# Optimization experiments

Measured on AMD Instinct MI355X. Metric: run time of the kernel, lower is better.

## Reference

```python
import jax, jax.numpy as jnp
import numpy as np

N_M = 100000  # musicians
N_T = 100000  # tracks
E = 400000
D = 128


def _sage(x_src, x_dst, edge, W_l, b_l, W_r, n_dst):
    """PyG SAGEConv: lin_l(mean_{j in N(i)} x_src[j]) + lin_r(x_dst[i])."""
    src, dst = edge[0], edge[1]
    msg = x_src[src]                                   # [E, D] gather
    agg = jax.ops.segment_sum(msg, dst, num_segments=n_dst)
    cnt = jax.ops.segment_sum(jnp.ones((edge.shape[1],), x_src.dtype), dst,
                              num_segments=n_dst)
    agg = agg / jnp.maximum(cnt, 1.0)[:, None]         # mean aggregation
    return agg @ W_l.T + b_l + x_dst @ W_r.T


def setup_inputs() -> dict:
    key = jax.random.key(0)
    ks = jax.random.split(key, 7)
    scale = 0.05
    return {
        "x_m": jax.random.normal(ks[0], (N_M, D), jnp.float32),
        "x_t": jax.random.normal(ks[1], (N_T, D), jnp.float32),
        "Wl": jax.random.normal(ks[2], (3, 2, D, D), jnp.float32) * scale,
        "bl": jnp.zeros((3, 2, D), jnp.float32),
        "Wr": jax.random.normal(ks[3], (3, 2, D, D), jnp.float32) * scale,
        "edge_mt": jax.random.randint(ks[4], (2, E), 0, N_T, jnp.int32).astype(jnp.int64),
        "edge_tm": jax.random.randint(ks[5], (2, E), 0, N_M, jnp.int32).astype(jnp.int64),
    }


def reference(x_m, x_t, Wl, bl, Wr, edge_mt, edge_tm):
    # 3 HeteroConv(SAGEConv) layers; dropout=0.0 is identity.
    for layer in range(3):
        # edge type 0: musician -plays_on-> track  (dst = track)
        new_t = _sage(x_m, x_t, edge_mt, Wl[layer, 0], bl[layer, 0], Wr[layer, 0], N_T)
        # edge type 1: track -features-> musician  (dst = musician)
        new_m = _sage(x_t, x_m, edge_tm, Wl[layer, 1], bl[layer, 1], Wr[layer, 1], N_M)
        if layer < 2:
            new_m = jax.nn.relu(new_m)
            new_t = jax.nn.relu(new_t)
        x_m, x_t = new_m, new_t
    return x_m, x_t
```

## Files before the change

kernel.cpp:

```cpp
#include <hip/hip_runtime.h>
#include <hip/hip_bf16.h>

typedef __bf16 bf16_t;
typedef __attribute__((ext_vector_type(4))) __bf16 bf16x4;
typedef __attribute__((ext_vector_type(8))) __bf16 bf16x8;
typedef __attribute__((ext_vector_type(4))) float f32x4;

#define DIM 128
#define GTILE 32

__device__ __forceinline__ void gl_lds16(const void* g, void* l) {
    __builtin_amdgcn_global_load_lds(
        (const __attribute__((address_space(1))) unsigned int*)g,
        (__attribute__((address_space(3))) unsigned int*)l, 16, 0, 0);
}

__global__ void prep_count(const float* __restrict__ Wl, const float* __restrict__ Wr,
                           bf16_t* __restrict__ Wc,
                           const int* __restrict__ dA, int* __restrict__ cA,
                           const int* __restrict__ dB, int* __restrict__ cB,
                           int E, int PB) {
    int blk = blockIdx.x;
    if (blk < PB) {
        int idx = blk * 256 + threadIdx.x;
        if (idx >= 6 * 128 * 256) return;
        int k = idx & 255;
        int n = (idx >> 8) & 127;
        int s = idx >> 15;
        float v;
        if (k < 128) v = Wl[((size_t)s * 128 + n) * 128 + k];
        else         v = Wr[((size_t)s * 128 + n) * 128 + (k - 128)];
        Wc[idx] = (bf16_t)v;
    } else {
        int i = (blk - PB) * 256 + threadIdx.x;
        if (i < E) atomicAdd(&cA[dA[i]], 1);
        else if (i < 2 * E) atomicAdd(&cB[dB[i - E]], 1);
    }
}

__global__ __launch_bounds__(256) void scan_local2(
    const int* __restrict__ cntA, int* __restrict__ partA, int* __restrict__ bsumA,
    int MA, int NBA,
    const int* __restrict__ cntB, int* __restrict__ partB, int* __restrict__ bsumB,
    int MB) {
    int blk = blockIdx.x;
    const int* cnt; int* partial; int* blocksum; int M; int b;
    if (blk < NBA) { cnt = cntA; partial = partA; blocksum = bsumA; M = MA; b = blk; }
    else           { cnt = cntB; partial = partB; blocksum = bsumB; M = MB; b = blk - NBA; }
    __shared__ int sdata[256];
    int i = b * 256 + threadIdx.x;
    int v = (i < M) ? cnt[i] : 0;
    sdata[threadIdx.x] = v;
    __syncthreads();
    for (int off = 1; off < 256; off <<= 1) {
        int t = (threadIdx.x >= off) ? sdata[threadIdx.x - off] : 0;
        __syncthreads();
        sdata[threadIdx.x] += t;
        __syncthreads();
    }
    int incl = sdata[threadIdx.x];
    if (i < M) partial[i] = incl - v;
    if (threadIdx.x == 255) blocksum[b] = incl;
}

__global__ __launch_bounds__(256) void scan_blocks2(int* __restrict__ bsA, int NA,
                                                    int* __restrict__ bsB, int NBcnt) {
    int* blocksum = blockIdx.x ? bsB : bsA;
    int NB = blockIdx.x ? NBcnt : NA;
    __shared__ int sdata[256];
    __shared__ int running;
    if (threadIdx.x == 0) running = 0;
    __syncthreads();
    for (int base = 0; base < NB; base += 256) {
        int i = base + threadIdx.x;
        int v = (i < NB) ? blocksum[i] : 0;
        sdata[threadIdx.x] = v;
        __syncthreads();
        for (int off = 1; off < 256; off <<= 1) {
            int t = (threadIdx.x >= off) ? sdata[threadIdx.x - off] : 0;
            __syncthreads();
            sdata[threadIdx.x] += t;
            __syncthreads();
        }
        int incl = sdata[threadIdx.x];
        int r = running;
        __syncthreads();
        if (i < NB) blocksum[i] = incl - v + r;
        if (threadIdx.x == 0) running = r + sdata[255];
        __syncthreads();
    }
}

__global__ __launch_bounds__(256) void add_offsets2(
    const int* __restrict__ pA, const int* __restrict__ bsA,
    int* __restrict__ rsA, int* __restrict__ curA, int MA, int NBA,
    const int* __restrict__ pB, const int* __restrict__ bsB,
    int* __restrict__ rsB, int* __restrict__ curB, int MB) {
    int blk = blockIdx.x;
    const int *partial, *blocksum; int *rowstart, *cursor; int M, b;
    if (blk < NBA) { partial = pA; blocksum = bsA; rowstart = rsA; cursor = curA; M = MA; b = blk; }
    else           { partial = pB; blocksum = bsB; rowstart = rsB; cursor = curB; M = MB; b = blk - NBA; }
    int i = b * 256 + threadIdx.x;
    if (i < M) {
        int rs = partial[i] + blocksum[i >> 8];
        rowstart[i] = rs;
        cursor[i] = rs;
    }
}

__global__ void bin_edges2(const int* __restrict__ sA, const int* __restrict__ dA,
                           int* __restrict__ curA, int* __restrict__ csrA,
                           const int* __restrict__ sB, const int* __restrict__ dB,
                           int* __restrict__ curB, int* __restrict__ csrB, int E) {
    int e = blockIdx.x * blockDim.x + threadIdx.x;
    if (e < E) {
        int d = dA[e];
        int pos = atomicAdd(&curA[d], 1);
        csrA[pos] = sA[e];
    } else if (e < 2 * E) {
        int i = e - E;
        int d = dB[i];
        int pos = atomicAdd(&curB[d], 1);
        csrB[pos] = sB[i];
    }
}

#define A0SZ 8192

template <int MODE>
__global__ __launch_bounds__(256, 3) void fused2(
    const void* __restrict__ gsA, const int* __restrict__ rsA,
    const int* __restrict__ cnA, const int* __restrict__ csA,
    const void* __restrict__ a1A, const bf16_t* __restrict__ WcA,
    const float* __restrict__ bA, void* __restrict__ oA, int Ma,
    const void* __restrict__ gsB, const int* __restrict__ rsB,
    const int* __restrict__ cnB, const int* __restrict__ csB,
    const void* __restrict__ a1B, const bf16_t* __restrict__ WcB,
    const float* __restrict__ bB, void* __restrict__ oB, int Mb) {
    constexpr int A1SZ = (MODE == 0) ? 16384 : 8192;
    __shared__ char smem[A0SZ + 2 * A1SZ];

    const int tid  = threadIdx.x;
    const int wid  = tid >> 6;
    const int lane = tid & 63;
    const int quad = lane >> 4;
    const int l16  = lane & 15;

    const int side = blockIdx.x & 1;
    const int t0   = blockIdx.x >> 1;
    const int gs   = gridDim.x >> 1;

    const void *gsrc, *a1p; const int *rsx, *cnx, *csx;
    const bf16_t* Wc; const float* bias; void* outp; int M;
    if (side == 0) { gsrc = gsA; rsx = rsA; cnx = cnA; csx = csA; a1p = a1A;
                     Wc = WcA; bias = bA; outp = oA; M = Ma; }
    else           { gsrc = gsB; rsx = rsB; cnx = cnB; csx = csB; a1p = a1B;
                     Wc = WcB; bias = bB; outp = oB; M = Mb; }
    const int nt = (M + GTILE - 1) / GTILE;
    if (t0 >= nt) return;

    bf16x8 breg[2][8];
#pragma unroll
    for (int ct = 0; ct < 2; ++ct)
#pragma unroll
        for (int kt = 0; kt < 8; ++kt)
            breg[ct][kt] = *(const bf16x8*)(
                Wc + (size_t)(wid * 32 + ct * 16 + l16) * 256 + kt * 32 + quad * 8);

    const float bcol0 = bias[wid * 32 + l16];
    const float bcol1 = bias[wid * 32 + 16 + l16];
    const int sw = l16 & 7;

    int s_row[4], s_off[4];
    if constexpr (MODE == 0) {
#pragma unroll
        for (int c = 0; c < 4; ++c) {
            int o = wid * 4096 + c * 1024 + lane * 16;
            int row = o >> 9;
            int ch  = (o >> 4) & 31;
            s_row[c] = row;
            s_off[c] = (ch ^ (row & 7)) * 4;
        }
    } else {
#pragma unroll
        for (int c = 0; c < 2; ++c) {
            int o = wid * 2048 + c * 1024 + lane * 16;
            int row = o >> 8;
            int ch  = (o >> 4) & 15;
            s_row[c] = row;
            s_off[c] = (ch ^ (row & 7)) * 8;
        }
    }

    auto STAGE = [&](int b, int t) {
        const int r0 = t * GTILE;
        char* base = smem + A0SZ + b * A1SZ;
        if constexpr (MODE == 0) {
            const float* A1f = (const float*)a1p;
#pragma unroll
            for (int c = 0; c < 4; ++c) {
                int grow = r0 + s_row[c]; if (grow >= M) grow = M - 1;
                gl_lds16(A1f + (size_t)grow * DIM + s_off[c],
                         base + wid * 4096 + c * 1024);
            }
        } else {
            const bf16_t* A1h = (const bf16_t*)a1p;
#pragma unroll
            for (int c = 0; c < 2; ++c) {
                int grow = r0 + s_row[c]; if (grow >= M) grow = M - 1;
                gl_lds16(A1h + (size_t)grow * DIM + s_off[c],
                         base + wid * 2048 + c * 1024);
            }
        }
    };

    auto GATHER = [&](int t) {
        const int hw  = tid >> 5;
        const int l32 = tid & 31;
        char* a0 = smem;
#pragma unroll 1
        for (int rr = 0; rr < 4; ++rr) {
            int r = hw * 4 + rr;
            int d = t * GTILE + r;
            float4 acc0 = {0.f, 0.f, 0.f, 0.f};
            float4 acc1 = {0.f, 0.f, 0.f, 0.f};
            int n = 0;
            if (d < M) {
                int start = rsx[d];
                n = cnx[d];
                for (int k = 0; k < n; k += 8) {
                    int sv[8];
#pragma unroll
                    for (int j = 0; j < 8; ++j)
                        sv[j] = csx[start + min(k + j, n - 1)];
                    float4 vv[8];
                    if constexpr (MODE == 0) {
                        const float* xg = (const float*)gsrc;
#pragma unroll
                        for (int j = 0; j < 8; ++j)
                            vv[j] = ((const float4*)(xg + (size_t)sv[j] * DIM))[l32];
                    } else {
                        const bf16_t* xg = (const bf16_t*)gsrc;
#pragma unroll
                        for (int j = 0; j < 8; ++j) {
                            bf16x4 b4 = *(const bf16x4*)(xg + (size_t)sv[j] * DIM + l32 * 4);
                            vv[j] = (float4){(float)b4[0], (float)b4[1],
                                             (float)b4[2], (float)b4[3]};
                        }
                    }
#pragma unroll
                    for (int j = 0; j < 8; j += 2) {
                        float w0 = (k + j     < n) ? 1.f : 0.f;
                        float w1 = (k + j + 1 < n) ? 1.f : 0.f;
                        acc0.x += vv[j].x * w0; acc0.y += vv[j].y * w0;
                        acc0.z += vv[j].z * w0; acc0.w += vv[j].w * w0;
                        acc1.x += vv[j + 1].x * w1; acc1.y += vv[j + 1].y * w1;
                        acc1.z += vv[j + 1].z * w1; acc1.w += vv[j + 1].w * w1;
                    }
                }
            }
            float invn = 1.0f / (float)max(n, 1);
            bf16x4 res;
            res[0] = (bf16_t)((acc0.x + acc1.x) * invn);
            res[1] = (bf16_t)((acc0.y + acc1.y) * invn);
            res[2] = (bf16_t)((acc0.z + acc1.z) * invn);
            res[3] = (bf16_t)((acc0.w + acc1.w) * invn);
            *(bf16x4*)(a0 + r * 256 + (((l32 >> 1) ^ (r & 7)) << 4) + ((l32 & 1) << 3)) = res;
        }
    };

    auto COMPUTE = [&](int b, int t) {
        const int r0 = t * GTILE;
        const char* a0base = smem;
        const char* a1base = smem + A0SZ + b * A1SZ;
        f32x4 acc[2][2];
#pragma unroll
        for (int rt = 0; rt < 2; ++rt) {
            acc[rt][0] = (f32x4){0.f, 0.f, 0.f, 0.f};
            acc[rt][1] = (f32x4){0.f, 0.f, 0.f, 0.f};
        }
#pragma unroll
        for (int rt = 0; rt < 2; ++rt) {
            const int row = rt * 16 + l16;
            bf16x8 alo[4];
#pragma unroll
            for (int kt = 0; kt < 4; ++kt)
                alo[kt] = *(const bf16x8*)(a0base + row * 256 + ((kt * 4 + quad) ^ sw) * 16);
#pragma unroll
            for (int kt = 0; kt < 4; ++kt) {
                acc[rt][0] = __builtin_amdgcn_mfma_f32_16x16x32_bf16(alo[kt], breg[0][kt], acc[rt][0], 0, 0, 0);
                acc[rt][1] = __builtin_amdgcn_mfma_f32_16x16x32_bf16(alo[kt], breg[1][kt], acc[rt][1], 0, 0, 0);
            }
            if constexpr (MODE == 0) {
#pragma unroll
                for (int kt = 0; kt < 4; ++kt) {
                    const int cc = kt * 8 + quad * 2;
                    float4 x0 = *(const float4*)(a1base + row * 512 + ((cc)     ^ sw) * 16);
                    float4 x1 = *(const float4*)(a1base + row * 512 + ((cc + 1) ^ sw) * 16);
                    bf16x8 ah;
                    ah[0] = (bf16_t)x0.x; ah[1] = (bf16_t)x0.y;
                    ah[2] = (bf16_t)x0.z; ah[3] = (bf16_t)x0.w;
                    ah[4] = (bf16_t)x1.x; ah[5] = (bf16_t)x1.y;
                    ah[6] = (bf16_t)x1.z; ah[7] = (bf16_t)x1.w;
                    acc[rt][0] = __builtin_amdgcn_mfma_f32_16x16x32_bf16(ah, breg[0][kt + 4], acc[rt][0], 0, 0, 0);
                    acc[rt][1] = __builtin_amdgcn_mfma_f32_16x16x32_bf16(ah, breg[1][kt + 4], acc[rt][1], 0, 0, 0);
                }
            } else {
#pragma unroll
                for (int kt = 0; kt < 4; ++kt) {
                    bf16x8 ah = *(const bf16x8*)(a1base + row * 256 + ((kt * 4 + quad) ^ sw) * 16);
                    acc[rt][0] = __builtin_amdgcn_mfma_f32_16x16x32_bf16(ah, breg[0][kt + 4], acc[rt][0], 0, 0, 0);
                    acc[rt][1] = __builtin_amdgcn_mfma_f32_16x16x32_bf16(ah, breg[1][kt + 4], acc[rt][1], 0, 0, 0);
                }
            }
        }
#pragma unroll
        for (int ct = 0; ct < 2; ++ct) {
            const int col = wid * 32 + ct * 16 + l16;
            const float bv = ct ? bcol1 : bcol0;
#pragma unroll
            for (int rt = 0; rt < 2; ++rt)
#pragma unroll
                for (int r = 0; r < 4; ++r) {
                    int row = r0 + rt * 16 + quad * 4 + r;
                    if (row < M) {
                        float v = acc[rt][ct][r] + bv;
                        if (MODE < 2) v = fmaxf(v, 0.f);
                        if constexpr (MODE == 2)
                            ((float*)outp)[(size_t)row * DIM + col] = v;
                        else
                            ((bf16_t*)outp)[(size_t)row * DIM + col] = (bf16_t)v;
                    }
                }
        }
    };

    STAGE(0, t0);
    int cur = 0;
    for (int t = t0; t < nt; t += gs, cur ^= 1) {
        const int nxt = t + gs;
        if (nxt < nt) STAGE(cur ^ 1, nxt);
        GATHER(t);
        __syncthreads();
        COMPUTE(cur, t);
        __syncthreads();
    }
}

extern "C" void kernel_launch(void* const* d_in, const int* in_sizes, int n_in,
                              void* d_out, int out_size, void* d_ws, size_t ws_size,
                              hipStream_t stream) {
    const float* x_m = (const float*)d_in[0];
    const float* x_t = (const float*)d_in[1];
    const float* Wl  = (const float*)d_in[2];
    const float* bl  = (const float*)d_in[3];
    const float* Wr  = (const float*)d_in[4];
    const int* e_mt  = (const int*)d_in[5];
    const int* e_tm  = (const int*)d_in[6];

    const int Mm = in_sizes[0] / DIM;
    const int Mt = in_sizes[1] / DIM;
    const int E  = in_sizes[5] / 2;
    const int NBt = (Mt + 255) / 256;
    const int NBm = (Mm + 255) / 256;

    float* out_m = (float*)d_out;
    float* out_t = (float*)d_out + (size_t)Mm * DIM;

    char* ws = (char*)d_ws;
    size_t off = 0;
    auto alloc = [&](size_t bytes) -> void* {
        void* p = ws + off;
        off += (bytes + 255) & ~(size_t)255;
        return p;
    };
    bf16_t* xb_m0  = (bf16_t*)alloc((size_t)Mm * DIM * 2);
    bf16_t* xb_t0  = (bf16_t*)alloc((size_t)Mt * DIM * 2);
    bf16_t* xb_m1  = (bf16_t*)alloc((size_t)Mm * DIM * 2);
    bf16_t* xb_t1  = (bf16_t*)alloc((size_t)Mt * DIM * 2);
    int*    cnt_t  = (int*)alloc((size_t)Mt * 4);
    int*    cnt_m  = (int*)alloc((size_t)Mm * 4);
    int*    rs_t   = (int*)alloc((size_t)Mt * 4);
    int*    rs_m   = (int*)alloc((size_t)Mm * 4);
    int*    cur_tb = (int*)alloc((size_t)Mt * 4);
    int*    cur_mb = (int*)alloc((size_t)Mm * 4);
    int*    part_t = (int*)alloc((size_t)Mt * 4);
    int*    part_m = (int*)alloc((size_t)Mm * 4);
    int*    bsum_t = (int*)alloc((size_t)NBt * 4);
    int*    bsum_m = (int*)alloc((size_t)NBm * 4);
    int*    csr_t  = (int*)alloc((size_t)E * 4);
    int*    csr_m  = (int*)alloc((size_t)E * 4);
    bf16_t* Wc     = (bf16_t*)alloc((size_t)6 * 128 * 256 * 2);

    hipMemsetAsync(cnt_t, 0, (size_t)Mt * 4, stream);
    hipMemsetAsync(cnt_m, 0, (size_t)Mm * 4, stream);

    const int PB = (6 * 128 * 256 + 255) / 256;
    const int CB = (2 * E + 255) / 256;
    prep_count<<<PB + CB, 256, 0, stream>>>(Wl, Wr, Wc, e_mt + E, cnt_t, e_tm + E, cnt_m, E, PB);

    scan_local2<<<NBt + NBm, 256, 0, stream>>>(cnt_t, part_t, bsum_t, Mt, NBt,
                                               cnt_m, part_m, bsum_m, Mm);
    scan_blocks2<<<2, 256, 0, stream>>>(bsum_t, NBt, bsum_m, NBm);
    add_offsets2<<<NBt + NBm, 256, 0, stream>>>(part_t, bsum_t, rs_t, cur_tb, Mt, NBt,
                                                part_m, bsum_m, rs_m, cur_mb, Mm);
    bin_edges2<<<(2 * E + 255) / 256, 256, 0, stream>>>(e_mt, e_mt + E, cur_tb, csr_t,
                                                        e_tm, e_tm + E, cur_mb, csr_m, E);

    int GG = 768;
    {
        int ntT = (Mt + GTILE - 1) / GTILE, ntM = (Mm + GTILE - 1) / GTILE;
        int need = 2 * ((ntT > ntM) ? ntT : ntM);
        if (GG > need) GG = need;
        GG &= ~1;
        if (GG < 2) GG = 2;
    }

    const float* biasT0 = bl + 0 * DIM;  const float* biasM0 = bl + 1 * DIM;
    const float* biasT1 = bl + 2 * DIM;  const float* biasM1 = bl + 3 * DIM;
    const float* biasT2 = bl + 4 * DIM;  const float* biasM2 = bl + 5 * DIM;
    const bf16_t* WcT0 = Wc + 0 * 128 * 256;  const bf16_t* WcM0 = Wc + 1 * 128 * 256;
    const bf16_t* WcT1 = Wc + 2 * 128 * 256;  const bf16_t* WcM1 = Wc + 3 * 128 * 256;
    const bf16_t* WcT2 = Wc + 4 * 128 * 256;  const bf16_t* WcM2 = Wc + 5 * 128 * 256;

    fused2<0><<<GG, 256, 0, stream>>>(
        x_m, rs_t, cnt_t, csr_t, x_t, WcT0, biasT0, xb_t0, Mt,
        x_t, rs_m, cnt_m, csr_m, x_m, WcM0, biasM0, xb_m0, Mm);
    fused2<1><<<GG, 256, 0, stream>>>(
        xb_m0, rs_t, cnt_t, csr_t, xb_t0, WcT1, biasT1, xb_t1, Mt,
        xb_t0, rs_m, cnt_m, csr_m, xb_m0, WcM1, biasM1, xb_m1, Mm);
    fused2<2><<<GG, 256, 0, stream>>>(
        xb_m1, rs_t, cnt_t, csr_t, xb_t1, WcT2, biasT2, out_t, Mt,
        xb_t1, rs_m, cnt_m, csr_m, xb_m1, WcM2, biasM2, out_m, Mm);
}
```

Measured before the change: 511.4 us.

## Pre-convert inputs to bf16 in prep kernel and unify layers on bf16 path

Adds a conversion stage to the prep kernel that casts x_m and x_t to bf16 buffers, so the first layer reads bf16 for both the gather and the self-term instead of fp32. That halves first-layer gather traffic and LDS footprint and removes the fp32 special-case code. With smaller LDS, launch bounds go from 3 to 5 blocks per CU and the grid grows from 768 to 1280. The cost is an extra full pass over both fp32 inputs before the fused kernels.

```diff
diff --git a/kernel.cpp b/kernel.cpp
--- a/kernel.cpp
+++ b/kernel.cpp
@@ -18,8 +18,10 @@
 __global__ void prep_count(const float* __restrict__ Wl, const float* __restrict__ Wr,
                            bf16_t* __restrict__ Wc,
                            const int* __restrict__ dA, int* __restrict__ cA,
-                           const int* __restrict__ dB, int* __restrict__ cB,
-                           int E, int PB) {
+                           const int* __restrict__ dB, int* __restrict__ cB, int E,
+                           const float* __restrict__ xm, bf16_t* __restrict__ xbm, int CM,
+                           const float* __restrict__ xt, bf16_t* __restrict__ xbt, int CT,
+                           int PB, int CB) {
     int blk = blockIdx.x;
     if (blk < PB) {
         int idx = blk * 256 + threadIdx.x;
@@ -31,10 +33,22 @@
         if (k < 128) v = Wl[((size_t)s * 128 + n) * 128 + k];
         else         v = Wr[((size_t)s * 128 + n) * 128 + (k - 128)];
         Wc[idx] = (bf16_t)v;
-    } else {
+    } else if (blk < PB + CB) {
         int i = (blk - PB) * 256 + threadIdx.x;
         if (i < E) atomicAdd(&cA[dA[i]], 1);
         else if (i < 2 * E) atomicAdd(&cB[dB[i - E]], 1);
+    } else {
+        int i = (blk - PB - CB) * 256 + threadIdx.x;
+        const float* src; bf16_t* dst;
+        if (i < CM) { src = xm; dst = xbm; }
+        else if ((i -= CM) < CT) { src = xt; dst = xbt; }
+        else return;
+        float4 a = ((const float4*)src)[(size_t)i * 2];
+        float4 b = ((const float4*)src)[(size_t)i * 2 + 1];
+        bf16x8 r;
+        r[0] = (bf16_t)a.x; r[1] = (bf16_t)a.y; r[2] = (bf16_t)a.z; r[3] = (bf16_t)a.w;
+        r[4] = (bf16_t)b.x; r[5] = (bf16_t)b.y; r[6] = (bf16_t)b.z; r[7] = (bf16_t)b.w;
+        *(bf16x8*)(dst + (size_t)i * 8) = r;
     }
 }
 
@@ -126,18 +140,18 @@
 }
 
 #define A0SZ 8192
+#define A1SZ 8192
 
 template <int MODE>
-__global__ __launch_bounds__(256, 3) void fused2(
-    const void* __restrict__ gsA, const int* __restrict__ rsA,
+__global__ __launch_bounds__(256, 5) void fused2(
+    const bf16_t* __restrict__ gsA, const int* __restrict__ rsA,
     const int* __restrict__ cnA, const int* __restrict__ csA,
-    const void* __restrict__ a1A, const bf16_t* __restrict__ WcA,
+    const bf16_t* __restrict__ a1A, const bf16_t* __restrict__ WcA,
     const float* __restrict__ bA, void* __restrict__ oA, int Ma,
-    const void* __restrict__ gsB, const int* __restrict__ rsB,
+    const bf16_t* __restrict__ gsB, const int* __restrict__ rsB,
     const int* __restrict__ cnB, const int* __restrict__ csB,
-    const void* __restrict__ a1B, const bf16_t* __restrict__ WcB,
+    const bf16_t* __restrict__ a1B, const bf16_t* __restrict__ WcB,
     const float* __restrict__ bB, void* __restrict__ oB, int Mb) {
-    constexpr int A1SZ = (MODE == 0) ? 16384 : 8192;
     __shared__ char smem[A0SZ + 2 * A1SZ];
 
     const int tid  = threadIdx.x;
@@ -150,7 +164,7 @@
     const int t0   = blockIdx.x >> 1;
     const int gs   = gridDim.x >> 1;
 
-    const void *gsrc, *a1p; const int *rsx, *cnx, *csx;
+    const bf16_t *gsrc, *a1p; const int *rsx, *cnx, *csx;
     const bf16_t* Wc; const float* bias; void* outp; int M;
     if (side == 0) { gsrc = gsA; rsx = rsA; cnx = cnA; csx = csA; a1p = a1A;
                      Wc = WcA; bias = bA; outp = oA; M = Ma; }
@@ -171,46 +185,24 @@
     const float bcol1 = bias[wid * 32 + 16 + l16];
     const int sw = l16 & 7;
 
-    int s_row[4], s_off[4];
-    if constexpr (MODE == 0) {
-#pragma unroll
-        for (int c = 0; c < 4; ++c) {
-            int o = wid * 4096 + c * 1024 + lane * 16;
-            int row = o >> 9;
-            int ch  = (o >> 4) & 31;
-            s_row[c] = row;
-            s_off[c] = (ch ^ (row & 7)) * 4;
-        }
-    } else {
-#pragma unroll
-        for (int c = 0; c < 2; ++c) {
-            int o = wid * 2048 + c * 1024 + lane * 16;
-            int row = o >> 8;
-            int ch  = (o >> 4) & 15;
-            s_row[c] = row;
-            s_off[c] = (ch ^ (row & 7)) * 8;
-        }
+    int s_row[2], s_off[2];
+#pragma unroll
+    for (int c = 0; c < 2; ++c) {
+        int o = wid * 2048 + c * 1024 + lane * 16;
+        int row = o >> 8;
+        int ch  = (o >> 4) & 15;
+        s_row[c] = row;
+        s_off[c] = (ch ^ (row & 7)) * 8;
     }
 
     auto STAGE = [&](int b, int t) {
         const int r0 = t * GTILE;
         char* base = smem + A0SZ + b * A1SZ;
-        if constexpr (MODE == 0) {
-            const float* A1f = (const float*)a1p;
-#pragma unroll
-            for (int c = 0; c < 4; ++c) {
-                int grow = r0 + s_row[c]; if (grow >= M) grow = M - 1;
-                gl_lds16(A1f + (size_t)grow * DIM + s_off[c],
-                         base + wid * 4096 + c * 1024);
-            }
-        } else {
-            const bf16_t* A1h = (const bf16_t*)a1p;
-#pragma unroll
-            for (int c = 0; c < 2; ++c) {
-                int grow = r0 + s_row[c]; if (grow >= M) grow = M - 1;
-                gl_lds16(A1h + (size_t)grow * DIM + s_off[c],
-                         base + wid * 2048 + c * 1024);
-            }
+#pragma unroll
+        for (int c = 0; c < 2; ++c) {
+            int grow = r0 + s_row[c]; if (grow >= M) grow = M - 1;
+            gl_lds16(a1p + (size_t)grow * DIM + s_off[c],
+                     base + wid * 2048 + c * 1024);
         }
     };
 
@@ -234,19 +226,11 @@
                     for (int j = 0; j < 8; ++j)
                         sv[j] = csx[start + min(k + j, n - 1)];
                     float4 vv[8];
-                    if constexpr (MODE == 0) {
-                        const float* xg = (const float*)gsrc;
-#pragma unroll
-                        for (int j = 0; j < 8; ++j)
-                            vv[j] = ((const float4*)(xg + (size_t)sv[j] * DIM))[l32];
-                    } else {
-                        const bf16_t* xg = (const bf16_t*)gsrc;
-#pragma unroll
-                        for (int j = 0; j < 8; ++j) {
-                            bf16x4 b4 = *(const bf16x4*)(xg + (size_t)sv[j] * DIM + l32 * 4);
-                            vv[j] = (float4){(float)b4[0], (float)b4[1],
-                                             (float)b4[2], (float)b4[3]};
-                        }
+#pragma unroll
+                    for (int j = 0; j < 8; ++j) {
+                        bf16x4 b4 = *(const bf16x4*)(gsrc + (size_t)sv[j] * DIM + l32 * 4);
+                        vv[j] = (float4){(float)b4[0], (float)b4[1],
+                                         (float)b4[2], (float)b4[3]};
                     }
 #pragma unroll
                     for (int j = 0; j < 8; j += 2) {
@@ -291,27 +275,11 @@
                 acc[rt][0] = __builtin_amdgcn_mfma_f32_16x16x32_bf16(alo[kt], breg[0][kt], acc[rt][0], 0, 0, 0);
                 acc[rt][1] = __builtin_amdgcn_mfma_f32_16x16x32_bf16(alo[kt], breg[1][kt], acc[rt][1], 0, 0, 0);
             }
-            if constexpr (MODE == 0) {
-#pragma unroll
-                for (int kt = 0; kt < 4; ++kt) {
-                    const int cc = kt * 8 + quad * 2;
-                    float4 x0 = *(const float4*)(a1base + row * 512 + ((cc)     ^ sw) * 16);
-                    float4 x1 = *(const float4*)(a1base + row * 512 + ((cc + 1) ^ sw) * 16);
-                    bf16x8 ah;
-                    ah[0] = (bf16_t)x0.x; ah[1] = (bf16_t)x0.y;
-                    ah[2] = (bf16_t)x0.z; ah[3] = (bf16_t)x0.w;
-                    ah[4] = (bf16_t)x1.x; ah[5] = (bf16_t)x1.y;
-                    ah[6] = (bf16_t)x1.z; ah[7] = (bf16_t)x1.w;
-                    acc[rt][0] = __builtin_amdgcn_mfma_f32_16x16x32_bf16(ah, breg[0][kt + 4], acc[rt][0], 0, 0, 0);
-                    acc[rt][1] = __builtin_amdgcn_mfma_f32_16x16x32_bf16(ah, breg[1][kt + 4], acc[rt][1], 0, 0, 0);
-                }
-            } else {
-#pragma unroll
-                for (int kt = 0; kt < 4; ++kt) {
-                    bf16x8 ah = *(const bf16x8*)(a1base + row * 256 + ((kt * 4 + quad) ^ sw) * 16);
-                    acc[rt][0] = __builtin_amdgcn_mfma_f32_16x16x32_bf16(ah, breg[0][kt + 4], acc[rt][0], 0, 0, 0);
-                    acc[rt][1] = __builtin_amdgcn_mfma_f32_16x16x32_bf16(ah, breg[1][kt + 4], acc[rt][1], 0, 0, 0);
-                }
+#pragma unroll
+            for (int kt = 0; kt < 4; ++kt) {
+                bf16x8 ah = *(const bf16x8*)(a1base + row * 256 + ((kt * 4 + quad) ^ sw) * 16);
+                acc[rt][0] = __builtin_amdgcn_mfma_f32_16x16x32_bf16(ah, breg[0][kt + 4], acc[rt][0], 0, 0, 0);
+                acc[rt][1] = __builtin_amdgcn_mfma_f32_16x16x32_bf16(ah, breg[1][kt + 4], acc[rt][1], 0, 0, 0);
             }
         }
 #pragma unroll
@@ -325,7 +293,7 @@
                     int row = r0 + rt * 16 + quad * 4 + r;
                     if (row < M) {
                         float v = acc[rt][ct][r] + bv;
-                        if (MODE < 2) v = fmaxf(v, 0.f);
+                        if (MODE == 1) v = fmaxf(v, 0.f);
                         if constexpr (MODE == 2)
                             ((float*)outp)[(size_t)row * DIM + col] = v;
                         else
@@ -374,6 +342,8 @@
         off += (bytes + 255) & ~(size_t)255;
         return p;
     };
+    bf16_t* xbm    = (bf16_t*)alloc((size_t)Mm * DIM * 2);
+    bf16_t* xbt    = (bf16_t*)alloc((size_t)Mt * DIM * 2);
     bf16_t* xb_m0  = (bf16_t*)alloc((size_t)Mm * DIM * 2);
     bf16_t* xb_t0  = (bf16_t*)alloc((size_t)Mt * DIM * 2);
     bf16_t* xb_m1  = (bf16_t*)alloc((size_t)Mm * DIM * 2);
@@ -395,9 +365,13 @@
     hipMemsetAsync(cnt_t, 0, (size_t)Mt * 4, stream);
     hipMemsetAsync(cnt_m, 0, (size_t)Mm * 4, stream);
 
+    const int CM = Mm * DIM / 8, CT = Mt * DIM / 8;
     const int PB = (6 * 128 * 256 + 255) / 256;
     const int CB = (2 * E + 255) / 256;
-    prep_count<<<PB + CB, 256, 0, stream>>>(Wl, Wr, Wc, e_mt + E, cnt_t, e_tm + E, cnt_m, E, PB);
+    const int XB = (CM + CT + 255) / 256;
+    prep_count<<<PB + CB + XB, 256, 0, stream>>>(Wl, Wr, Wc,
+                                                 e_mt + E, cnt_t, e_tm + E, cnt_m, E,
+                                                 x_m, xbm, CM, x_t, xbt, CT, PB, CB);
 
     scan_local2<<<NBt + NBm, 256, 0, stream>>>(cnt_t, part_t, bsum_t, Mt, NBt,
                                                cnt_m, part_m, bsum_m, Mm);
@@ -407,7 +381,7 @@
     bin_edges2<<<(2 * E + 255) / 256, 256, 0, stream>>>(e_mt, e_mt + E, cur_tb, csr_t,
                                                         e_tm, e_tm + E, cur_mb, csr_m, E);
 
-    int GG = 768;
+    int GG = 1280;
     {
         int ntT = (Mt + GTILE - 1) / GTILE, ntM = (Mm + GTILE - 1) / GTILE;
         int need = 2 * ((ntT > ntM) ? ntT : ntM);
@@ -423,9 +397,9 @@
     const bf16_t* WcT1 = Wc + 2 * 128 * 256;  const bf16_t* WcM1 = Wc + 3 * 128 * 256;
     const bf16_t* WcT2 = Wc + 4 * 128 * 256;  const bf16_t* WcM2 = Wc + 5 * 128 * 256;
 
-    fused2<0><<<GG, 256, 0, stream>>>(
-        x_m, rs_t, cnt_t, csr_t, x_t, WcT0, biasT0, xb_t0, Mt,
-        x_t, rs_m, cnt_m, csr_m, x_m, WcM0, biasM0, xb_m0, Mm);
+    fused2<1><<<GG, 256, 0, stream>>>(
+        xbm, rs_t, cnt_t, csr_t, xbt, WcT0, biasT0, xb_t0, Mt,
+        xbt, rs_m, cnt_m, csr_m, xbm, WcM0, biasM0, xb_m0, Mm);
     fused2<1><<<GG, 256, 0, stream>>>(
         xb_m0, rs_t, cnt_t, csr_t, xb_t0, WcT1, biasT1, xb_t1, Mt,
         xb_t0, rs_m, cnt_m, csr_m, xb_m0, WcM1, biasM1, xb_m1, Mm);
```

Measured after the change: 716.4 us. 40.1% more time.
